# Optimization experiments

Hardware: AMD Instinct MI355X
Metric: run time of the kernel (lower is better)

The kernel has to match this reference:

```python
import math
import jax, jax.numpy as jnp
import numpy as np

B, N, M, C, H = 64, 64, 64, 512, 8
HD = C // H
FREQ = 256  # frequency_embedding_size
MAX_PERIOD = 10000.0


def setup_inputs() -> dict:
    key = jax.random.key(0)
    ks = jax.random.split(key, 10)
    s = 1.0 / math.sqrt(C)
    sf = 1.0 / math.sqrt(FREQ)
    return {
        "query": jax.random.normal(ks[0], (B, N, C), jnp.float32),
        "query_pos": jax.random.uniform(ks[1], (1, N, M), jnp.float32),
        # projection weights stored as [in, out]
        "Wq": jax.random.normal(ks[2], (C, C), jnp.float32) * s,
        "bq": jnp.zeros((C,), jnp.float32),
        "Wk": jax.random.normal(ks[3], (C, C), jnp.float32) * s,  # no bias
        "Wv": jax.random.normal(ks[4], (C, C), jnp.float32) * s,
        "bv": jnp.zeros((C,), jnp.float32),
        "Wo": jax.random.normal(ks[5], (C, C), jnp.float32) * s,
        "bo": jnp.zeros((C,), jnp.float32),
        # ScalarEmbedder MLP: Linear(FREQ->C), SiLU, Linear(C->C)
        "W1": jax.random.normal(ks[6], (FREQ, C), jnp.float32) * sf,
        "b1": jnp.zeros((C,), jnp.float32),
        "W2": jax.random.normal(ks[7], (C, C), jnp.float32) * s,
        "b2": jnp.zeros((C,), jnp.float32),
    }


def _freqs():
    half = FREQ // 2
    return jnp.exp(-math.log(MAX_PERIOD) * jnp.arange(half, dtype=jnp.float32) / half)


def reference(query, query_pos, Wq, bq, Wk, Wv, bv, Wo, bo, W1, b1, W2, b2):
    Bq, Nq, Cq = query.shape
    Mk = query_pos.shape[-1]
    # --- ScalarEmbedder on flattened pairwise positions: [N*M] -> [N*M, C]
    t = query_pos.reshape(-1)                       # [Bp*N*M], Bp = 1
    tf = t[:, None] * _freqs()[None, :]             # [N*M, FREQ/2]
    emb = jnp.concatenate([jnp.cos(tf), jnp.sin(tf)], axis=-1)  # [N*M, FREQ]
    pe = jax.nn.silu(emb @ W1 + b1) @ W2 + b2        # [N*M, C]
    pe = pe.reshape(Nq, Mk, H, HD).transpose(2, 0, 1, 3)  # [H, N, M, hd] (tiled over B via broadcast)

    q = (query @ Wq + bq).reshape(Bq, Nq, H, HD)     # bnhd
    k = (query @ Wk).reshape(Bq, Mk, H, HD)          # bmhd (key = query)
    v = (query @ Wv + bv).reshape(Bq, Mk, H, HD)

    scale = HD ** -0.5
    # attn[b,h,n,m] = sum_d q[b,n,h,d] * pe[h,n,m,d] * k[b,m,h,d]
    scores = jnp.einsum("bnhd,hnmd,bmhd->bhnm", q, pe, k) * scale
    attn = jax.nn.softmax(scores, axis=-1)
    x = jnp.einsum("bhnm,bmhd->bnhd", attn, v).reshape(Bq, Nq, Cq)
    return x @ Wo + bo + query  # identity = query
```

## Files before the change

kernel.cpp:

```cpp
#include <hip/hip_runtime.h>
#include <hip/hip_bf16.h>
#include <math.h>

typedef short short8 __attribute__((ext_vector_type(8)));
typedef float floatx4 __attribute__((ext_vector_type(4)));

__device__ __forceinline__ ushort f2bf(float f) {
    __hip_bfloat16 h = __float2bfloat16(f);
    return *reinterpret_cast<ushort*>(&h);
}
__device__ __forceinline__ void bf8_to_f32(uint4 u, float* f) {
    f[0] = __uint_as_float(u.x << 16); f[1] = __uint_as_float(u.x & 0xffff0000u);
    f[2] = __uint_as_float(u.y << 16); f[3] = __uint_as_float(u.y & 0xffff0000u);
    f[4] = __uint_as_float(u.z << 16); f[5] = __uint_as_float(u.z & 0xffff0000u);
    f[6] = __uint_as_float(u.w << 16); f[7] = __uint_as_float(u.w & 0xffff0000u);
}

#define GLDS16(g, l) __builtin_amdgcn_global_load_lds( \
    (const __attribute__((address_space(1))) void*)(g), \
    (__attribute__((address_space(3))) void*)(l), 16, 0, 0)

__global__ __launch_bounds__(256) void prep_kernel(
        const float* __restrict__ W1, const float* __restrict__ W2,
        const float* __restrict__ Wq, const float* __restrict__ Wk,
        const float* __restrict__ Wv, const float* __restrict__ Wo,
        const float* __restrict__ bq, const float* __restrict__ bv,
        const float* __restrict__ query, const float* __restrict__ qpos,
        ushort* __restrict__ W1t, ushort* __restrict__ W2t,
        ushort* __restrict__ Wqkvt, ushort* __restrict__ Wot,
        ushort* __restrict__ queryB, ushort* __restrict__ embB,
        float* __restrict__ biasC) {
    const int z = blockIdx.z;
    const int tx = threadIdx.x, ty = threadIdx.y;
    const int tid = ty * 32 + tx;
    if (z < 6) {
        const float* src; ushort* dst; int R;
        switch (z) {
            case 0:  src = W1; dst = W1t;              R = 256; break;
            case 1:  src = W2; dst = W2t;              R = 512; break;
            case 2:  src = Wq; dst = Wqkvt;            R = 512; break;
            case 3:  src = Wk; dst = Wqkvt + 512*512;  R = 512; break;
            case 4:  src = Wv; dst = Wqkvt + 1024*512; R = 512; break;
            default: src = Wo; dst = Wot;              R = 512; break;
        }
        const int r0 = blockIdx.y * 32, c0 = blockIdx.x * 32;
        if (r0 >= R) return;
        __shared__ float t[32][33];
        for (int i = ty; i < 32; i += 8) t[i][tx] = src[(size_t)(r0 + i) * 512 + c0 + tx];
        __syncthreads();
        for (int i = ty; i < 32; i += 8) dst[(size_t)(c0 + i) * R + r0 + tx] = f2bf(t[tx][i]);
    } else if (z == 6) {
        const int bid = blockIdx.y * 16 + blockIdx.x;
#pragma unroll
        for (int i = 0; i < 8; ++i) {
            size_t idx4 = (size_t)bid * 2048 + i * 256 + tid;
            float4 v = *(const float4*)(query + idx4 * 4);
            ushort4 o; o.x = f2bf(v.x); o.y = f2bf(v.y); o.z = f2bf(v.z); o.w = f2bf(v.w);
            *(ushort4*)(queryB + idx4 * 4) = o;
        }
        if (bid == 0) {
            for (int i = tid; i < 1536; i += 256)
                biasC[i] = (i < 512) ? bq[i] : ((i < 1024) ? 0.0f : bv[i - 1024]);
        }
    } else {
        const int bid = blockIdx.y * 16 + blockIdx.x;
        const int gt = bid * 256 + tid;
        const int r = gt >> 4;
        const int j0 = (gt & 15) * 8;
        const float t = qpos[r];
        ushort oc[8], os[8];
#pragma unroll
        for (int u = 0; u < 8; ++u) {
            int i = j0 + u;
            float freq = __expf(-9.210340371976184f * (float)i * (1.0f / 128.0f));
            float a = t * freq;
            oc[u] = f2bf(__cosf(a));
            os[u] = f2bf(__sinf(a));
        }
        *(uint4*)(embB + r * 256 + j0)       = *(uint4*)&oc[0];
        *(uint4*)(embB + r * 256 + j0 + 128) = *(uint4*)&os[0];
    }
}

struct GArgs {
    const ushort* A; const ushort* Bt; const float* bias; const float* resid;
    void* C; int N, K, act, outf32, ntn;
};

template<int BM, int BN>
__global__ __launch_bounds__(256) void gemm_multi(GArgs g0, GArgs g1, int split) {
    constexpr int MR = BM / 32;
    constexpr int NR = BN / 32;
    constexpr int NLOADS = (BM / 64 + BN / 64) * 2;
    __shared__ ushort As[2][2][BM * 32];
    __shared__ ushort Bs[2][2][BN * 32];

    const bool sel = ((int)blockIdx.x >= split);
    const GArgs g = sel ? g1 : g0;
    const int bid = sel ? ((int)blockIdx.x - split) : (int)blockIdx.x;
    const int tm = bid / g.ntn, tn = bid % g.ntn;
    const int row0 = tm * BM, col0 = tn * BN;
    const int K = g.K, N = g.N;

    const int tid = threadIdx.x;
    const int l = tid & 63, w = tid >> 6;
    const int wr = w >> 1, wc = w & 1;
    const int l15 = l & 15, quad = l >> 4;

    const int srow = tid >> 2;
    const int skoff = (tid & 3) * 8;
    const ushort* gA = g.A  + (size_t)(row0 + srow) * K + skoff;
    const ushort* gB = g.Bt + (size_t)(col0 + srow) * K + skoff;

    auto stage = [&](int s, int k0) {
#pragma unroll
        for (int p = 0; p < 2; ++p) {
#pragma unroll
            for (int i = 0; i < BM / 64; ++i)
                GLDS16(gA + (size_t)(i * 64) * K + k0 + p * 32, &As[s][p][(i * 256 + tid) * 8]);
#pragma unroll
            for (int i = 0; i < BN / 64; ++i)
                GLDS16(gB + (size_t)(i * 64) * K + k0 + p * 32, &Bs[s][p][(i * 256 + tid) * 8]);
        }
    };

    floatx4 acc[MR][NR] = {};

    const int nk = K >> 6;
    stage(0, 0);
    int cur = 0;
    for (int t = 0; t < nk; ++t) {
        if (t + 1 < nk) {
            stage(cur ^ 1, (t + 1) * 64);
            asm volatile("s_waitcnt vmcnt(%0)" :: "i"(NLOADS) : "memory");
        } else {
            asm volatile("s_waitcnt vmcnt(0)" ::: "memory");
        }
        __builtin_amdgcn_s_barrier();
#pragma unroll
        for (int ks = 0; ks < 2; ++ks) {
            short8 af[MR], bf[NR];
#pragma unroll
            for (int m = 0; m < MR; ++m)
                af[m] = *(const short8*)&As[cur][ks][(wr * (BM / 2) + m * 16 + l15) * 32 + quad * 8];
#pragma unroll
            for (int n = 0; n < NR; ++n)
                bf[n] = *(const short8*)&Bs[cur][ks][(wc * (BN / 2) + n * 16 + l15) * 32 + quad * 8];
#pragma unroll
            for (int m = 0; m < MR; ++m)
#pragma unroll
                for (int n = 0; n < NR; ++n)
                    acc[m][n] = __builtin_amdgcn_mfma_f32_16x16x32_bf16(af[m], bf[n], acc[m][n], 0, 0, 0);
        }
        asm volatile("s_waitcnt lgkmcnt(0)" ::: "memory");
        __builtin_amdgcn_s_barrier();
        cur ^= 1;
    }

#pragma unroll
    for (int m = 0; m < MR; ++m)
#pragma unroll
        for (int n = 0; n < NR; ++n) {
            int col = col0 + wc * (BN / 2) + n * 16 + l15;
            float bvv = g.bias ? g.bias[col] : 0.0f;
#pragma unroll
            for (int r = 0; r < 4; ++r) {
                int row = row0 + wr * (BM / 2) + m * 16 + quad * 4 + r;
                float val = acc[m][n][r] + bvv;
                if (g.act) val = val / (1.0f + __expf(-val));
                if (g.outf32) {
                    float rv = g.resid ? g.resid[(size_t)row * N + col] : 0.0f;
                    ((float*)g.C)[(size_t)row * N + col] = val + rv;
                } else {
                    ((ushort*)g.C)[(size_t)row * N + col] = f2bf(val);
                }
            }
        }
}

__global__ __launch_bounds__(256) void attn_bf16(
        const ushort* __restrict__ qkv, const ushort* __restrict__ peB,
        ushort* __restrict__ xB) {
    constexpr int PT = 72;
    const int h = blockIdx.x, b = blockIdx.y, nq = blockIdx.z;
    const int tid = threadIdx.x;
    const int w = tid >> 6, l = tid & 63;
    const int lo = l & 7, hi = l >> 3;
    const int l15 = l & 15, quad = l >> 4;

    __shared__ ushort vsT[64 * PT];
    __shared__ ushort ps[16 * PT];

    {
        const int rp = tid >> 3, ch = tid & 7;
        const ushort* vb = qkv + (size_t)(b * 64 + 2 * rp) * 1536 + h * 64 + 1024 + ch * 8;
        uint4 v0 = *(const uint4*)vb;
        uint4 v1 = *(const uint4*)(vb + 1536);
        const ushort* a0 = (const ushort*)&v0;
        const ushort* a1 = (const ushort*)&v1;
#pragma unroll
        for (int j = 0; j < 8; ++j) {
            uint pk = (uint)a0[j] | ((uint)a1[j] << 16);
            *(uint*)&vsT[(ch * 8 + j) * PT + 2 * rp] = pk;
        }
    }

    short8 ku[8];
#pragma unroll
    for (int mg = 0; mg < 8; ++mg)
        ku[mg] = *(const short8*)(qkv + (size_t)(b * 64 + mg * 8 + hi) * 1536 + h * 64 + 512 + lo * 8);

#pragma unroll
    for (int i = 0; i < 4; ++i) {
        int nl = w + 4 * i;
        int n = nq * 16 + nl;

        uint4 qu = *(const uint4*)(qkv + (size_t)(b * 64 + n) * 1536 + h * 64 + lo * 8);
        float qf[8]; bf8_to_f32(qu, qf);

        uint4 pu[8];
#pragma unroll
        for (int mg = 0; mg < 8; ++mg)
            pu[mg] = *(const uint4*)(peB + (size_t)(n * 64 + mg * 8 + hi) * 512 + h * 64 + lo * 8);

        float sreg[8];
#pragma unroll
        for (int mg = 0; mg < 8; ++mg) {
            float pf[8]; bf8_to_f32(pu[mg], pf);
            const ushort* kk = (const ushort*)&ku[mg];
            float p = 0.0f;
#pragma unroll
            for (int j = 0; j < 8; ++j) {
                float kfj = __uint_as_float(((uint)kk[j]) << 16);
                p = fmaf(qf[j] * kfj, pf[j], p);
            }
            p += __shfl_xor(p, 1);
            p += __shfl_xor(p, 2);
            p += __shfl_xor(p, 4);
            sreg[mg] = p * 0.125f;
        }

        float sum = 0.0f;
#pragma unroll
        for (int mg = 0; mg < 8; ++mg) { sreg[mg] = __expf(sreg[mg]); sum += sreg[mg]; }
        sum += __shfl_xor(sum, 8);
        sum += __shfl_xor(sum, 16);
        sum += __shfl_xor(sum, 32);
        float rs = 1.0f / sum;

        float pv = sreg[0];
#pragma unroll
        for (int mg = 1; mg < 8; ++mg) if (lo == mg) pv = sreg[mg];
        ps[nl * PT + 8 * lo + hi] = f2bf(pv * rs);
    }
    __syncthreads();

    {
        const int dt = w;
        floatx4 o0 = {0.f, 0.f, 0.f, 0.f};
#pragma unroll
        for (int ks = 0; ks < 2; ++ks) {
            short8 a  = *(const short8*)&ps[l15 * PT + ks * 32 + quad * 8];
            short8 b0 = *(const short8*)&vsT[(dt * 16 + l15) * PT + ks * 32 + quad * 8];
            o0 = __builtin_amdgcn_mfma_f32_16x16x32_bf16(a, b0, o0, 0, 0, 0);
        }
        const int nbase = nq * 16 + quad * 4;
#pragma unroll
        for (int r = 0; r < 4; ++r) {
            size_t rowoff = (size_t)(b * 64 + nbase + r) * 512 + h * 64;
            xB[rowoff + dt * 16 + l15] = f2bf(o0[r]);
        }
    }
}

extern "C" void kernel_launch(void* const* d_in, const int* in_sizes, int n_in,
                              void* d_out, int out_size, void* d_ws, size_t ws_size,
                              hipStream_t stream) {
    const float* query = (const float*)d_in[0];
    const float* qpos  = (const float*)d_in[1];
    const float* Wq    = (const float*)d_in[2];
    const float* bq    = (const float*)d_in[3];
    const float* Wk    = (const float*)d_in[4];
    const float* Wv    = (const float*)d_in[5];
    const float* bv    = (const float*)d_in[6];
    const float* Wo    = (const float*)d_in[7];
    const float* bo    = (const float*)d_in[8];
    const float* W1    = (const float*)d_in[9];
    const float* b1    = (const float*)d_in[10];
    const float* W2    = (const float*)d_in[11];
    const float* b2    = (const float*)d_in[12];
    float* out = (float*)d_out;
    char* ws = (char*)d_ws;

    ushort* W1t    = (ushort*)(ws + 0);
    ushort* W2t    = (ushort*)(ws + 262144);
    ushort* Wqkvt  = (ushort*)(ws + 786432);
    ushort* Wot    = (ushort*)(ws + 2359296);
    float*  biasC  = (float*) (ws + 2883584);
    ushort* embB   = (ushort*)(ws + 3145728);
    ushort* queryB = (ushort*)(ws + 5242880);
    ushort* hiddenB= (ushort*)(ws + 9437184);
    ushort* peB    = (ushort*)(ws + 13631488);
    ushort* qkvB   = (ushort*)(ws + 17825792);
    ushort* xB     = (ushort*)(ws + 30408704);

    prep_kernel<<<dim3(16, 16, 8), dim3(32, 8), 0, stream>>>(
        W1, W2, Wq, Wk, Wv, Wo, bq, bv, query, qpos,
        W1t, W2t, Wqkvt, Wot, queryB, embB, biasC);

    GArgs a_g1 { embB,    W1t,   b1,    nullptr, hiddenB, 512,  256, 1, 0, 8  };
    GArgs a_g2 { hiddenB, W2t,   b2,    nullptr, peB,     512,  512, 0, 0, 8  };
    GArgs a_qkv{ queryB,  Wqkvt, biasC, nullptr, qkvB,    1536, 512, 0, 0, 24 };
    GArgs a_out{ xB,      Wot,   bo,    query,   out,     512,  512, 0, 1, 8  };

    gemm_multi<64, 64><<<512, 256, 0, stream>>>(a_g1, a_g1, 1 << 30);
    gemm_multi<64, 64><<<2048, 256, 0, stream>>>(a_g2, a_qkv, 512);

    attn_bf16<<<dim3(8, 64, 4), 256, 0, stream>>>(qkvB, peB, xB);

    gemm_multi<64, 64><<<512, 256, 0, stream>>>(a_out, a_out, 1 << 30);
}
```

Baseline: 150.3 us.

## Stage K tile in LDS and halve PE register buffering in attention kernel

The attention kernel no longer keeps all eight K fragments in registers. K is staged into a 64x64 shared-memory tile and read back per group, and the positional-embedding loads are split into two batches of four instead of eight. A launch bound requesting 8 blocks per CU is added. The aim is lower VGPR pressure and higher occupancy, which helps hide the latency of the large PE reads. In exchange it adds an extra barrier and LDS traffic, and the two-batch split reduces memory-level parallelism within each wave.

Result: no change. 151.1 us (+0.5%).

```diff
diff --git a/kernel.cpp b/kernel.cpp
--- a/kernel.cpp
+++ b/kernel.cpp
@@ -178,7 +178,7 @@
         }
 }
 
-__global__ __launch_bounds__(256) void attn_bf16(
+__global__ __launch_bounds__(256, 8) void attn_bf16(
         const ushort* __restrict__ qkv, const ushort* __restrict__ peB,
         ushort* __restrict__ xB) {
     constexpr int PT = 72;
@@ -188,9 +188,18 @@
     const int lo = l & 7, hi = l >> 3;
     const int l15 = l & 15, quad = l >> 4;
 
+    __shared__ ushort kls[64 * 64];
     __shared__ ushort vsT[64 * PT];
     __shared__ ushort ps[16 * PT];
 
+    {
+        const int row = tid >> 2, c4 = tid & 3;
+        const ushort* kb = qkv + (size_t)(b * 64 + row) * 1536 + h * 64 + 512 + c4 * 16;
+        uint4 k0 = *(const uint4*)kb;
+        uint4 k1 = *(const uint4*)(kb + 8);
+        *(uint4*)&kls[row * 64 + c4 * 16]     = k0;
+        *(uint4*)&kls[row * 64 + c4 * 16 + 8] = k1;
+    }
     {
         const int rp = tid >> 3, ch = tid & 7;
         const ushort* vb = qkv + (size_t)(b * 64 + 2 * rp) * 1536 + h * 64 + 1024 + ch * 8;
@@ -204,11 +213,7 @@
             *(uint*)&vsT[(ch * 8 + j) * PT + 2 * rp] = pk;
         }
     }
-
-    short8 ku[8];
-#pragma unroll
-    for (int mg = 0; mg < 8; ++mg)
-        ku[mg] = *(const short8*)(qkv + (size_t)(b * 64 + mg * 8 + hi) * 1536 + h * 64 + 512 + lo * 8);
+    __syncthreads();
 
 #pragma unroll
     for (int i = 0; i < 4; ++i) {
@@ -218,26 +223,32 @@
         uint4 qu = *(const uint4*)(qkv + (size_t)(b * 64 + n) * 1536 + h * 64 + lo * 8);
         float qf[8]; bf8_to_f32(qu, qf);
 
-        uint4 pu[8];
-#pragma unroll
-        for (int mg = 0; mg < 8; ++mg)
-            pu[mg] = *(const uint4*)(peB + (size_t)(n * 64 + mg * 8 + hi) * 512 + h * 64 + lo * 8);
-
         float sreg[8];
 #pragma unroll
-        for (int mg = 0; mg < 8; ++mg) {
-            float pf[8]; bf8_to_f32(pu[mg], pf);
-            const ushort* kk = (const ushort*)&ku[mg];
-            float p = 0.0f;
-#pragma unroll
-            for (int j = 0; j < 8; ++j) {
-                float kfj = __uint_as_float(((uint)kk[j]) << 16);
-                p = fmaf(qf[j] * kfj, pf[j], p);
+        for (int half = 0; half < 2; ++half) {
+            uint4 pu[4];
+#pragma unroll
+            for (int u = 0; u < 4; ++u) {
+                int mg = half * 4 + u;
+                pu[u] = *(const uint4*)(peB + (size_t)(n * 64 + mg * 8 + hi) * 512 + h * 64 + lo * 8);
             }
-            p += __shfl_xor(p, 1);
-            p += __shfl_xor(p, 2);
-            p += __shfl_xor(p, 4);
-            sreg[mg] = p * 0.125f;
+#pragma unroll
+            for (int u = 0; u < 4; ++u) {
+                int mg = half * 4 + u;
+                float pf[8]; bf8_to_f32(pu[u], pf);
+                short8 kk = *(const short8*)&kls[(mg * 8 + hi) * 64 + lo * 8];
+                const ushort* kp = (const ushort*)&kk;
+                float p = 0.0f;
+#pragma unroll
+                for (int j = 0; j < 8; ++j) {
+                    float kfj = __uint_as_float(((uint)kp[j]) << 16);
+                    p = fmaf(qf[j] * kfj, pf[j], p);
+                }
+                p += __shfl_xor(p, 1);
+                p += __shfl_xor(p, 2);
+                p += __shfl_xor(p, 4);
+                sreg[mg] = p * 0.125f;
+            }
         }
 
         float sum = 0.0f;
```
